# Performance work log

Measured on AMD Instinct MI355X. Metric: run time of the kernel, lower is better.

Reference implementation:

```python
import jax, jax.numpy as jnp
import numpy as np

N_VOCAB = 50400
D_MODEL = 4096
SHARDS = 8
SEQ = 2048
BATCH = 2
PER_IN = N_VOCAB // SHARDS      # 6300 vocab rows per shard
PER_OUT = D_MODEL // SHARDS     # 512 pos-emb dims per shard


def setup_inputs() -> dict:
    key = jax.random.key(0)
    k1, k2, k3, k4 = jax.random.split(key, 4)
    x = jax.random.randint(k1, (BATCH, SEQ), 0, N_VOCAB, dtype=jnp.int32)
    # Dense kernel [n_vocab, d_model] (vocab-sharded in the original) and bias [d_model]
    kernel = jax.random.truncated_normal(k2, -2.0, 2.0, (N_VOCAB, D_MODEL), dtype=jnp.float32) / np.sqrt(N_VOCAB)
    bias = jnp.zeros((D_MODEL,), dtype=jnp.float32)
    # per-shard positional embeddings, stacked as the all_gather result [shards, seq, per_out]
    pos_embs = 0.02 * jax.random.truncated_normal(k3, -2.0, 2.0, (SHARDS, SEQ, PER_OUT), dtype=jnp.float32)
    return {"x": x, "kernel": kernel, "bias": bias, "pos_embs": pos_embs}


def reference(x, kernel, bias, pos_embs):
    # Each shard s computes one_hot(clip(x - s*PER_IN, 0, PER_IN-1)) @ kernel_s + bias,
    # then psum over shards. Equivalent math via clipped gather into the full kernel:
    starts = jnp.arange(SHARDS, dtype=x.dtype) * PER_IN                 # [S]
    local = jnp.clip(x[None, :, :] - starts[:, None, None], 0, PER_IN - 1)
    gidx = local + starts[:, None, None]                                 # [S, B, T] global rows
    emb = kernel[gidx].sum(axis=0)                                       # [B, T, D] psum over shards
    emb = emb + jnp.asarray(SHARDS, bias.dtype) * bias                   # bias summed by psum S times
    # all_gather(pos_embs) -> [S, seq, per_out]; reshape(seq, -1) as in the original
    all_pos = pos_embs.reshape(SEQ, -1)                                  # [seq, d_model]
    return emb + all_pos[None, :, :]                                     # [B, T, D]
```

## Files before the change

### kernel.cpp

```cpp
#include <hip/hip_runtime.h>

#define N_VOCAB 50400
#define D_MODEL 4096
#define SHARDS  8
#define SEQ     2048
#define BATCH   2
#define PER_IN  6300

__global__ void boundary_sums_kernel(const float* __restrict__ kern,
                                     const float* __restrict__ bias,
                                     float* __restrict__ bsum) {
    int d = blockIdx.x * blockDim.x + threadIdx.x;
    if (d >= D_MODEL) return;
    float first[SHARDS], last[SHARDS];
#pragma unroll
    for (int s = 0; s < SHARDS; ++s) {
        first[s] = kern[(size_t)(s * PER_IN) * D_MODEL + d];
        last[s]  = kern[(size_t)(s * PER_IN + PER_IN - 1) * D_MODEL + d];
    }
    float b8 = (float)SHARDS * bias[d];
#pragma unroll
    for (int s = 0; s < SHARDS; ++s) {
        float acc = b8;
#pragma unroll
        for (int sp = 0; sp < SHARDS; ++sp) {
            if (sp < s)      acc += last[sp];
            else if (sp > s) acc += first[sp];
        }
        bsum[s * D_MODEL + d] = acc;
    }
}

__global__ __launch_bounds__(256)
void embed_gather_kernel(const int* __restrict__ x,
                         const float* __restrict__ kern,
                         const float* __restrict__ pos,
                         const float* __restrict__ bsum,
                         float* __restrict__ out) {
    const int token = blockIdx.x;
    const int t     = token & (SEQ - 1);
    const int tid   = threadIdx.x;

    const int row = x[token];
    const int s   = row / PER_IN;

    const float4* __restrict__ krow = (const float4*)(kern + (size_t)row * D_MODEL);
    const float4* __restrict__ prow = (const float4*)(pos  + (size_t)t   * D_MODEL);
    const float4* __restrict__ brow = (const float4*)(bsum + (size_t)s   * D_MODEL);
    float4* __restrict__       orow = (float4*)(out + (size_t)token * D_MODEL);

#pragma unroll
    for (int k = 0; k < (D_MODEL / 4) / 256; ++k) {
        const int i = tid + k * 256;
        float4 a = krow[i];
        float4 p = prow[i];
        float4 b = brow[i];
        float4 o;
        o.x = a.x + b.x + p.x;
        o.y = a.y + b.y + p.y;
        o.z = a.z + b.z + p.z;
        o.w = a.w + b.w + p.w;
        orow[i] = o;
    }
}

extern "C" void kernel_launch(void* const* d_in, const int* in_sizes, int n_in,
                              void* d_out, int out_size, void* d_ws, size_t ws_size,
                              hipStream_t stream) {
    const int*   x    = (const int*)  d_in[0];
    const float* kern = (const float*)d_in[1];
    const float* bias = (const float*)d_in[2];
    const float* pos  = (const float*)d_in[3];

    float* out  = (float*)d_out;
    float* bsum = (float*)d_ws;

    boundary_sums_kernel<<<(D_MODEL + 255) / 256, 256, 0, stream>>>(kern, bias, bsum);

    embed_gather_kernel<<<BATCH * SEQ, 256, 0, stream>>>(x, kern, pos, bsum, out);
}
```

Before: 39.30 us.

## Process both batch tokens per block, batch all loads, use nontemporal stores

After: 34.39 us. -12.5%, faster.

```diff
diff --git a/kernel.cpp b/kernel.cpp
--- a/kernel.cpp
+++ b/kernel.cpp
@@ -6,6 +6,8 @@
 #define SEQ     2048
 #define BATCH   2
 #define PER_IN  6300
+
+typedef float f4 __attribute__((ext_vector_type(4)));
 
 __global__ void boundary_sums_kernel(const float* __restrict__ kern,
                                      const float* __restrict__ bias,
@@ -37,30 +39,39 @@
                          const float* __restrict__ pos,
                          const float* __restrict__ bsum,
                          float* __restrict__ out) {
-    const int token = blockIdx.x;
-    const int t     = token & (SEQ - 1);
-    const int tid   = threadIdx.x;
+    const int t   = blockIdx.x;
+    const int tid = threadIdx.x;
 
-    const int row = x[token];
-    const int s   = row / PER_IN;
+    const int row0 = x[t];
+    const int row1 = x[SEQ + t];
+    const int s0 = row0 / PER_IN;
+    const int s1 = row1 / PER_IN;
 
-    const float4* __restrict__ krow = (const float4*)(kern + (size_t)row * D_MODEL);
-    const float4* __restrict__ prow = (const float4*)(pos  + (size_t)t   * D_MODEL);
-    const float4* __restrict__ brow = (const float4*)(bsum + (size_t)s   * D_MODEL);
-    float4* __restrict__       orow = (float4*)(out + (size_t)token * D_MODEL);
+    const f4* __restrict__ k0 = (const f4*)(kern + (size_t)row0 * D_MODEL);
+    const f4* __restrict__ k1 = (const f4*)(kern + (size_t)row1 * D_MODEL);
+    const f4* __restrict__ pr = (const f4*)(pos  + (size_t)t    * D_MODEL);
+    const f4* __restrict__ b0 = (const f4*)(bsum + (size_t)s0   * D_MODEL);
+    const f4* __restrict__ b1 = (const f4*)(bsum + (size_t)s1   * D_MODEL);
+    f4* __restrict__ o0 = (f4*)(out + (size_t)t         * D_MODEL);
+    f4* __restrict__ o1 = (f4*)(out + (size_t)(SEQ + t) * D_MODEL);
 
+    f4 a0[4], a1[4], pv[4], v0[4], v1[4];
 #pragma unroll
-    for (int k = 0; k < (D_MODEL / 4) / 256; ++k) {
+    for (int k = 0; k < 4; ++k) {
         const int i = tid + k * 256;
-        float4 a = krow[i];
-        float4 p = prow[i];
-        float4 b = brow[i];
-        float4 o;
-        o.x = a.x + b.x + p.x;
-        o.y = a.y + b.y + p.y;
-        o.z = a.z + b.z + p.z;
-        o.w = a.w + b.w + p.w;
-        orow[i] = o;
+        a0[k] = k0[i];
+        a1[k] = k1[i];
+        pv[k] = pr[i];
+        v0[k] = b0[i];
+        v1[k] = b1[i];
+    }
+#pragma unroll
+    for (int k = 0; k < 4; ++k) {
+        const int i = tid + k * 256;
+        f4 r0 = a0[k] + v0[k] + pv[k];
+        f4 r1 = a1[k] + v1[k] + pv[k];
+        __builtin_nontemporal_store(r0, &o0[i]);
+        __builtin_nontemporal_store(r1, &o1[i]);
     }
 }
 
@@ -77,5 +88,5 @@
 
     boundary_sums_kernel<<<(D_MODEL + 255) / 256, 256, 0, stream>>>(kern, bias, bsum);
 
-    embed_gather_kernel<<<BATCH * SEQ, 256, 0, stream>>>(x, kern, pos, bsum, out);
+    embed_gather_kernel<<<SEQ, 256, 0, stream>>>(x, kern, pos, bsum, out);
 }
```
